# Kernel optimization log

Hardware: AMD Instinct MI355X
Metric: run time of the kernel (lower is better)

The kernel has to match this reference:

```python
import jax, jax.numpy as jnp
import numpy as np

N, E, H, HEADS, HD, L = 4096, 65536, 128, 4, 32, 4
NF, GF, EF, B = 16, 8, 4, 1


def _ln(x, g, b, eps=1e-5):
    mu = x.mean(-1, keepdims=True)
    v = ((x - mu) ** 2).mean(-1, keepdims=True)
    return (x - mu) * jax.lax.rsqrt(v + eps) * g + b


def _lin(x, W, b=None):
    y = x @ W.T
    return y if b is None else y + b


def _gelu(x):
    return jax.nn.gelu(x, approximate=False)


def setup_inputs() -> dict:
    key = jax.random.key(0)
    ks = iter(jax.random.split(key, 64))
    def rn(shape, s=0.05):
        return jax.random.normal(next(ks), shape, jnp.float32) * s
    inp = {}
    inp['x'] = jax.random.normal(next(ks), (N, NF), jnp.float32)
    inp['edge_index'] = jax.random.randint(next(ks), (2, E), 0, N, dtype=jnp.int32)
    inp['edge_attr'] = jax.random.normal(next(ks), (E, EF), jnp.float32)
    inp['u'] = jax.random.normal(next(ks), (1, GF), jnp.float32)
    inp['acting_mask'] = jax.random.randint(next(ks), (N,), 0, 2, dtype=jnp.int32).astype(bool)
    inp['h_tiles'] = jnp.zeros((N, H), jnp.float32)
    inp['batch'] = jnp.zeros((N,), jnp.int32)
    inp['turn_frac'] = jax.random.uniform(next(ks), (1,), jnp.float32)
    # node / global encoders
    inp['ne_W'] = rn((H, NF + 1)); inp['ne_b'] = jnp.zeros((H,)); inp['ne_g'] = jnp.ones((H,)); inp['ne_be'] = jnp.zeros((H,))
    inp['ge_W'] = rn((H, GF)); inp['ge_b'] = jnp.zeros((H,)); inp['ge_g'] = jnp.ones((H,)); inp['ge_be'] = jnp.zeros((H,))
    # GRUCell
    inp['gru_Wih'] = rn((3 * H, H)); inp['gru_bih'] = jnp.zeros((3 * H,))
    inp['gru_Whh'] = rn((3 * H, H)); inp['gru_bhh'] = jnp.zeros((3 * H,))
    # stacked GATv2 layers
    inp['gat_Wl'] = rn((L, H, H)); inp['gat_bl'] = jnp.zeros((L, H))
    inp['gat_Wr'] = rn((L, H, H)); inp['gat_br'] = jnp.zeros((L, H))
    inp['gat_We'] = rn((L, H, EF))
    inp['gat_att'] = rn((L, HEADS, HD))
    inp['gat_bias'] = jnp.zeros((L, H))
    inp['ln_g'] = jnp.ones((L, H)); inp['ln_b'] = jnp.zeros((L, H))
    # global MHA
    inp['attn_Win'] = rn((3 * H, H)); inp['attn_bin'] = jnp.zeros((3 * H,))
    inp['attn_Wout'] = rn((H, H)); inp['attn_bout'] = jnp.zeros((H,))
    inp['lng_g'] = jnp.ones((H,)); inp['lng_b'] = jnp.zeros((H,))
    # heads (edge_in = 2H + EF)
    inp['mv_W1'] = rn((H, 2 * H + EF)); inp['mv_b1'] = jnp.zeros((H,))
    inp['mv_W2'] = rn((1, H)); inp['mv_b2'] = jnp.zeros((1,))
    inp['fr_W1'] = rn((H, 2 * H + EF)); inp['fr_b1'] = jnp.zeros((H,))
    inp['fr_W2'] = rn((2, H)); inp['fr_b2'] = jnp.zeros((2,))
    inp['vl_W1'] = rn((H, 2 * H)); inp['vl_b1'] = jnp.zeros((H,))
    inp['vl_W2'] = rn((1, H)); inp['vl_b2'] = jnp.zeros((1,))
    return inp


def reference(x, edge_index, edge_attr, u, acting_mask, h_tiles, batch, turn_frac,
              ne_W, ne_b, ne_g, ne_be, ge_W, ge_b, ge_g, ge_be,
              gru_Wih, gru_bih, gru_Whh, gru_bhh,
              gat_Wl, gat_bl, gat_Wr, gat_br, gat_We, gat_att, gat_bias, ln_g, ln_b,
              attn_Win, attn_bin, attn_Wout, attn_bout, lng_g, lng_b,
              mv_W1, mv_b1, mv_W2, mv_b2, fr_W1, fr_b1, fr_W2, fr_b2,
              vl_W1, vl_b1, vl_W2, vl_b2):
    Nn = x.shape[0]
    src, dst = edge_index[0], edge_index[1]
    xa = jnp.concatenate([x, jnp.broadcast_to(turn_frac, (Nn, 1))], -1)
    h = _gelu(_ln(_lin(xa, ne_W, ne_b), ne_g, ne_be))
    ue = _gelu(_ln(_lin(u, ge_W, ge_b), ge_g, ge_be))
    h = h + ue[batch]
    # GRUCell (torch semantics)
    gi = _lin(h, gru_Wih, gru_bih)
    gh = _lin(h_tiles, gru_Whh, gru_bhh)
    i_r, i_z, i_n = jnp.split(gi, 3, -1)
    h_r, h_z, h_n = jnp.split(gh, 3, -1)
    r = jax.nn.sigmoid(i_r + h_r)
    z = jax.nn.sigmoid(i_z + h_z)
    n = jnp.tanh(i_n + r * h_n)
    h = (1.0 - z) * n + z * h_tiles
    h_tiles_new = jax.lax.stop_gradient(h)
    # stacked GATv2 message passing (eval mode: no dropout)
    for l in range(L):
        xl = _lin(h, gat_Wl[l], gat_bl[l]).reshape(Nn, HEADS, HD)   # source messages
        xr = _lin(h, gat_Wr[l], gat_br[l]).reshape(Nn, HEADS, HD)   # target
        ee = (edge_attr @ gat_We[l].T).reshape(-1, HEADS, HD)
        m = xl[src]                                                 # [E,heads,hd]
        s = jax.nn.leaky_relu(m + xr[dst] + ee, negative_slope=0.2)
        score = (s * gat_att[l]).sum(-1)                            # [E,heads]
        mx = jax.ops.segment_max(score, dst, num_segments=Nn)
        mx = jnp.where(jnp.isfinite(mx), mx, 0.0)
        ex = jnp.exp(score - mx[dst])
        den = jax.ops.segment_sum(ex, dst, num_segments=Nn)
        alpha_e = ex / (den[dst] + 1e-16)
        agg = jax.ops.segment_sum(alpha_e[..., None] * m, dst, num_segments=Nn)
        h_mp = agg.reshape(Nn, H) + gat_bias[l]
        h = _ln(h + h_mp, ln_g[l], ln_b[l])
    # global self-attention over all nodes as one sequence
    q, k, v = jnp.split(_lin(h, attn_Win, attn_bin), 3, -1)
    q = q.reshape(Nn, HEADS, HD); k = k.reshape(Nn, HEADS, HD); v = v.reshape(Nn, HEADS, HD)
    att = jax.nn.softmax(jnp.einsum('nhd,mhd->hnm', q, k) / np.float32(np.sqrt(HD)), axis=-1)
    ao = jnp.einsum('hnm,mhd->nhd', att, v).reshape(Nn, H)
    h = _ln(h + _lin(ao, attn_Wout, attn_bout), lng_g, lng_b)
    # edge heads
    eemb = jnp.concatenate([h[src], h[dst], edge_attr], -1)         # [E, 2H+EF]
    move_logits = _lin(_gelu(_lin(eemb, mv_W1, mv_b1)), mv_W2, mv_b2)[:, 0]
    fp = _lin(_gelu(_lin(eemb, fr_W1, fr_b1)), fr_W2, fr_b2)
    alpha = jax.nn.softplus(fp[:, 0]) + 1e-4
    beta = jax.nn.softplus(fp[:, 1]) + 1e-4
    # value head (global mean pool + masked acting pool)
    cnt = jax.ops.segment_sum(jnp.ones((Nn, 1), h.dtype), batch, num_segments=B)
    gpool = jax.ops.segment_sum(h, batch, num_segments=B) / cnt
    ah = jnp.where(acting_mask[:, None], h, 0.0)
    asum = jax.ops.segment_sum(ah, batch, num_segments=B) / cnt
    acnt = jnp.maximum(jax.ops.segment_sum(acting_mask[:, None].astype(h.dtype), batch, num_segments=B) / cnt, 1e-6)
    apool = asum / acnt
    vin = jnp.concatenate([gpool, apool], -1)
    value = _lin(_gelu(_lin(vin, vl_W1, vl_b1)), vl_W2, vl_b2)[:, 0]
    return move_logits, alpha, beta, value, h_tiles_new
```

## Files before the change

kernel.cpp:

```cpp
#include <hip/hip_runtime.h>
#include <math.h>


#define NN 4096
#define EE 65536
#define HH 128
#define NHEADS 4
#define HDIM 32
#define NLAYERS 4
#define NFEAT 16
#define GFEAT 8
#define EFEAT 4
#define KS 4
#define KPAD 296
#define XSTR 136
#define KSTR 40
#define VSTR 136

typedef short bf16x8 __attribute__((ext_vector_type(8)));
typedef float f32x4  __attribute__((ext_vector_type(4)));
union UB { uint4 u; bf16x8 v; };

__device__ __forceinline__ float gelu_f(float x){
  return 0.5f * x * (1.0f + erff(x * 0.7071067811865475f));
}
__device__ __forceinline__ float gelu_fast(float x){
  float u = x + 0.044715f * x * x * x;
  float t = __expf(-1.5957691216f * u);
  return x / (1.0f + t);
}
__device__ __forceinline__ float sigm_fast(float x){ return 1.0f / (1.0f + __expf(-x)); }
__device__ __forceinline__ float tanh_fast(float x){
  float t = __expf(-2.0f * fmaxf(x, -40.0f));
  return 1.0f - 2.0f * t / (1.0f + t);
}
__device__ __forceinline__ float softplus_f(float x){ return x > 20.0f ? x : log1pf(expf(x)); }
__device__ __forceinline__ unsigned short f2bf(float x){
  unsigned u = __float_as_uint(x);
  unsigned r = (u + 0x7FFFu + ((u >> 16) & 1u)) >> 16;
  return (unsigned short)r;
}
__device__ __forceinline__ float bf2f(unsigned short x){
  return __uint_as_float(((unsigned)x) << 16);
}
__device__ __forceinline__ unsigned pack2bf(float lo, float hi){
  unsigned a = (__float_as_uint(lo) + 0x8000u) >> 16;
  unsigned b = (__float_as_uint(hi) + 0x8000u) & 0xFFFF0000u;
  return a | b;
}

__device__ __forceinline__ float block_sum128(float v, float* red){
  int j = threadIdx.x;
  red[j] = v; __syncthreads();
  for (int s = 64; s > 0; s >>= 1){
    if (j < s) red[j] += red[j + s];
    __syncthreads();
  }
  float r = red[0];
  __syncthreads();
  return r;
}

__global__ void k_hist(const int* __restrict__ ei, int* __restrict__ cnt){
  int e = blockIdx.x * 256 + threadIdx.x;
  if (e < EE) atomicAdd(&cnt[ei[EE + e]], 1);
}

__global__ void k_scan(const int* __restrict__ cnt, int* __restrict__ off, int* __restrict__ cur){
  __shared__ int part[256];
  int t = threadIdx.x;
  int local[16];
  int s = 0;
  #pragma unroll
  for (int i = 0; i < 16; i++){ local[i] = s; s += cnt[t * 16 + i]; }
  part[t] = s; __syncthreads();
  for (int o = 1; o < 256; o <<= 1){
    int v = (t >= o) ? part[t - o] : 0;
    __syncthreads();
    part[t] += v;
    __syncthreads();
  }
  int base = part[t] - s;
  #pragma unroll
  for (int i = 0; i < 16; i++){ int o = base + local[i]; off[t * 16 + i] = o; cur[t * 16 + i] = o; }
  if (t == 255) off[NN] = part[255];
}

__global__ void k_scatter(const int* __restrict__ ei, const float* __restrict__ ea,
                          int* __restrict__ cur,
                          int* __restrict__ srcs, float* __restrict__ eas4){
  int e = blockIdx.x * 256 + threadIdx.x;
  if (e < EE){
    int d = ei[EE + e];
    int p = atomicAdd(&cur[d], 1);
    srcs[p] = ei[e];
    float4 a = *(const float4*)(ea + e * 4);
    *(float4*)(eas4 + p * 4) = a;
  }
}

__global__ void k_wprep(const float* __restrict__ Wih, const float* __restrict__ Whh,
                        const float* __restrict__ Wl, const float* __restrict__ Wr,
                        const float* __restrict__ Win, const float* __restrict__ Wout,
                        const float* __restrict__ tiles,
                        const float* __restrict__ bl, const float* __restrict__ br,
                        const float* __restrict__ ea,
                        const float* __restrict__ mvW1, const float* __restrict__ frW1,
                        unsigned short* __restrict__ wbuf, unsigned short* __restrict__ tilesb,
                        float* __restrict__ blrc,
                        unsigned short* __restrict__ wbE, unsigned short* __restrict__ eab,
                        int* __restrict__ cnt, float* __restrict__ gsum){
  int i = blockIdx.x * 256 + threadIdx.x;
  if (i < 49152){ wbuf[i] = f2bf(Wih[i]); }
  else if (i < 98304){ int j = i - 49152; wbuf[49152 + j] = f2bf(Whh[j]); }
  else if (i < 229376){
    int j = i - 98304;
    int l = j >> 15, rem = j & 32767, m = rem >> 7, k = rem & 127;
    float v = (m < 128) ? Wl[l * 16384 + m * 128 + k] : Wr[l * 16384 + (m - 128) * 128 + k];
    wbuf[98304 + j] = f2bf(v);
  }
  else if (i < 278528){ int j = i - 229376; wbuf[229376 + j] = f2bf(Win[j]); }
  else if (i < 294912){ int j = i - 278528; wbuf[278528 + j] = f2bf(Wout[j]); }
  else if (i < 819200){ int j = i - 294912; tilesb[j] = f2bf(tiles[j]); }
  else if (i < 820224){
    int j = i - 819200;
    int l = j >> 8, m = j & 255;
    blrc[j] = (m < 128) ? bl[l * 128 + m] : br[l * 128 + m - 128];
  }
  else if (i < 896000){
    int j = i - 820224;
    int n = j / KPAD, k = j - n * KPAD;
    float v = 0.0f;
    if (k < 2 * HH + EFEAT) v = (n < HH) ? mvW1[n * (2 * HH + EFEAT) + k]
                                         : frW1[(n - HH) * (2 * HH + EFEAT) + k];
    wbE[j] = f2bf(v);
  }
  else if (i < 1158144){
    int j = i - 896000;
    eab[j] = f2bf(ea[j]);
  }
  else if (i < 1162240){ cnt[i - 1158144] = 0; }
  else if (i < 1162497){ gsum[i - 1162240] = 0.0f; }
}

__device__ __forceinline__ void gemm_core(const unsigned short* __restrict__ Xb, int n0,
                                          const unsigned short* __restrict__ Wb, int m0,
                                          unsigned short* Xs, f32x4 acc[8]){
  int t = threadIdx.x;
  #pragma unroll
  for (int k2 = 0; k2 < 4; k2++){
    int v = t + k2 * 256;
    int r = v >> 4, c8 = v & 15;
    *(uint4*)(Xs + r * XSTR + c8 * 8) = *(const uint4*)(Xb + (n0 + r) * 128 + c8 * 8);
  }
  __syncthreads();
  int ln = t & 63, w = t >> 6, lm = ln & 15, quad = ln >> 4;
  const unsigned short* abase = Xs + (16 * w + lm) * XSTR + quad * 8;
  const unsigned short* bbase = Wb + (m0 + lm) * 128 + quad * 8;
  UB af[4];
  #pragma unroll
  for (int ks = 0; ks < 4; ks++) af[ks].u = *(const uint4*)(abase + ks * 32);
  #pragma unroll
  for (int i = 0; i < 8; i++) acc[i] = (f32x4){0.f, 0.f, 0.f, 0.f};
  #pragma unroll
  for (int t2 = 0; t2 < 8; t2++){
    #pragma unroll
    for (int ks = 0; ks < 4; ks++){
      UB bu;
      bu.u = *(const uint4*)(bbase + t2 * 16 * 128 + ks * 32);
      acc[t2] = __builtin_amdgcn_mfma_f32_16x16x32_bf16(af[ks].v, bu.v, acc[t2], 0, 0, 0);
    }
  }
}

__global__ __launch_bounds__(256) void k_gru_lin(const unsigned short* __restrict__ hb,
                                                 const unsigned short* __restrict__ tilesb,
                                                 const unsigned short* __restrict__ Wihb,
                                                 const unsigned short* __restrict__ Whhb,
                                                 const float* __restrict__ bih,
                                                 const float* __restrict__ bhh,
                                                 float* __restrict__ gi, float* __restrict__ gh){
  __shared__ __align__(16) unsigned short Xs[64 * XSTR];
  int z = blockIdx.z;
  const unsigned short* Xb = z ? tilesb : hb;
  const unsigned short* Wb = z ? Whhb : Wihb;
  const float* bias = z ? bhh : bih;
  float* Y = z ? gh : gi;
  int t = threadIdx.x;
  int n0 = blockIdx.x * 64, m0 = blockIdx.y * 128;
  f32x4 acc[8];
  gemm_core(Xb, n0, Wb, m0, Xs, acc);
  int ln = t & 63, w = t >> 6, lm = ln & 15, quad = ln >> 4;
  #pragma unroll
  for (int t2 = 0; t2 < 8; t2++){
    float bv = bias[m0 + t2 * 16 + lm];
    #pragma unroll
    for (int r = 0; r < 4; r++){
      Y[(n0 + 16 * w + quad * 4 + r) * 384 + m0 + t2 * 16 + lm] = acc[t2][r] + bv;
    }
  }
}

__global__ __launch_bounds__(256) void k_lin_gat(const unsigned short* __restrict__ Xb,
                                                 const unsigned short* __restrict__ Wb,
                                                 const float* __restrict__ bias,
                                                 unsigned short* __restrict__ Y){
  __shared__ __align__(16) unsigned short Xs[64 * XSTR];
  int t = threadIdx.x;
  int n0 = blockIdx.x * 64, m0 = blockIdx.y * 128;
  f32x4 acc[8];
  gemm_core(Xb, n0, Wb, m0, Xs, acc);
  int ln = t & 63, w = t >> 6, lm = ln & 15, quad = ln >> 4;
  #pragma unroll
  for (int t2 = 0; t2 < 8; t2++){
    float bv = bias[m0 + t2 * 16 + lm];
    #pragma unroll
    for (int r = 0; r < 4; r++){
      Y[(n0 + 16 * w + quad * 4 + r) * 256 + m0 + t2 * 16 + lm] = f2bf(acc[t2][r] + bv);
    }
  }
}

__global__ __launch_bounds__(256) void k_lin_qkv(const unsigned short* __restrict__ Xb,
                                                 const unsigned short* __restrict__ Wb,
                                                 const float* __restrict__ bias,
                                                 unsigned short* __restrict__ qb,
                                                 unsigned short* __restrict__ kb,
                                                 unsigned short* __restrict__ vt){
  __shared__ __align__(16) unsigned short Xs[64 * XSTR];
  int t = threadIdx.x;
  int n0 = blockIdx.x * 64, m0 = blockIdx.y * 128;
  f32x4 acc[8];
  gemm_core(Xb, n0, Wb, m0, Xs, acc);
  int ln = t & 63, w = t >> 6, lm = ln & 15, quad = ln >> 4;
  int nb = n0 + 16 * w + quad * 4;
  const float scale = 0.17677669529663687f;
  if (blockIdx.y == 0){
    #pragma unroll
    for (int t2 = 0; t2 < 8; t2++){
      int m = t2 * 16 + lm;
      float bv = bias[m];
      #pragma unroll
      for (int r = 0; r < 4; r++) qb[(nb + r) * HH + m] = f2bf(acc[t2][r] + bv);
    }
  } else if (blockIdx.y == 1){
    #pragma unroll
    for (int t2 = 0; t2 < 8; t2++){
      int m = t2 * 16 + lm;
      float bv = bias[128 + m];
      #pragma unroll
      for (int r = 0; r < 4; r++) kb[(nb + r) * HH + m] = f2bf((acc[t2][r] + bv) * scale);
    }
  } else {
    #pragma unroll
    for (int t2 = 0; t2 < 8; t2++){
      int m = t2 * 16 + lm;
      float bv = bias[256 + m];
      uint2 p;
      p.x = pack2bf(acc[t2][0] + bv, acc[t2][1] + bv);
      p.y = pack2bf(acc[t2][2] + bv, acc[t2][3] + bv);
      *(uint2*)(vt + m * NN + nb) = p;
    }
  }
}

__global__ void k_node_enc(const float* __restrict__ x, const float* __restrict__ tf,
                           const float* __restrict__ W, const float* __restrict__ b,
                           const float* __restrict__ g, const float* __restrict__ be,
                           const float* __restrict__ u, const float* __restrict__ geW,
                           const float* __restrict__ geb, const float* __restrict__ geg,
                           const float* __restrict__ gebe,
                           float* __restrict__ h, unsigned short* __restrict__ hb){
  __shared__ float red[128];
  __shared__ float xs[NFEAT + 1];
  __shared__ float us[GFEAT];
  int n = blockIdx.x, j = threadIdx.x;
  if (j < NFEAT) xs[j] = x[n * NFEAT + j];
  if (j == NFEAT) xs[NFEAT] = tf[0];
  if (j >= 32 && j < 32 + GFEAT) us[j - 32] = u[j - 32];
  __syncthreads();
  float ua = geb[j];
  #pragma unroll
  for (int k = 0; k < GFEAT; k++) ua += us[k] * geW[j * GFEAT + k];
  float umu = block_sum128(ua, red) * (1.0f / HH);
  float ud = ua - umu;
  float uvar = block_sum128(ud * ud, red) * (1.0f / HH);
  float uej = gelu_f(ud * rsqrtf(uvar + 1e-5f) * geg[j] + gebe[j]);
  float acc = b[j];
  #pragma unroll
  for (int k = 0; k < NFEAT + 1; k++) acc += xs[k] * W[j * (NFEAT + 1) + k];
  float mu = block_sum128(acc, red) * (1.0f / HH);
  float d = acc - mu;
  float var = block_sum128(d * d, red) * (1.0f / HH);
  float r = gelu_f(d * rsqrtf(var + 1e-5f) * g[j] + be[j]) + uej;
  h[n * HH + j] = r;
  hb[n * HH + j] = f2bf(r);
}

__global__ void k_gru_comb(const float* __restrict__ gi, const float* __restrict__ gh,
                           const float* __restrict__ tiles, float* __restrict__ h,
                           unsigned short* __restrict__ hb, float* __restrict__ out_tiles){
  int idx = blockIdx.x * 256 + threadIdx.x;
  int n = idx >> 7, j = idx & 127;
  float ir = gi[n * 384 + j], iz = gi[n * 384 + 128 + j], inn = gi[n * 384 + 256 + j];
  float hr = gh[n * 384 + j], hz = gh[n * 384 + 128 + j], hn = gh[n * 384 + 256 + j];
  float r = sigm_fast(ir + hr), z = sigm_fast(iz + hz);
  float nn2 = tanh_fast(inn + r * hn);
  float ts = tiles[idx];
  float hnew = (1.0f - z) * nn2 + z * ts;
  h[idx] = hnew;
  hb[idx] = f2bf(hnew);
  out_tiles[idx] = hnew;
}

__global__ __launch_bounds__(256) void k_gat_agg(
    const unsigned short* __restrict__ xlrb,
    const int* __restrict__ off, const int* __restrict__ srcs,
    const float* __restrict__ eas4,
    const float* __restrict__ We, const float* __restrict__ att,
    const float* __restrict__ bias, const float* __restrict__ g,
    const float* __restrict__ b, float* __restrict__ h,
    unsigned short* __restrict__ hb){
  int t = threadIdx.x, w = t >> 6, j = t & 63;
  int n = blockIdx.x * 4 + w;
  int p0 = off[n], p1 = off[n + 1];
  int c0 = 2 * j;
  float4 w0 = ((const float4*)We)[c0];
  float4 w1 = ((const float4*)We)[c0 + 1];
  float at0 = att[c0], at1 = att[c0 + 1];
  unsigned xr = *(const unsigned*)(xlrb + n * 256 + 128 + c0);
  float xr0 = bf2f((unsigned short)xr), xr1 = bf2f((unsigned short)(xr >> 16));
  float den = 0.f, a0 = 0.f, a1 = 0.f;
  int p = p0;
  for (; p + 4 <= p1; p += 4){
    int s0 = srcs[p], s1 = srcs[p + 1], s2 = srcs[p + 2], s3 = srcs[p + 3];
    unsigned x0 = *(const unsigned*)(xlrb + s0 * 256 + c0);
    unsigned x1 = *(const unsigned*)(xlrb + s1 * 256 + c0);
    unsigned x2 = *(const unsigned*)(xlrb + s2 * 256 + c0);
    unsigned x3 = *(const unsigned*)(xlrb + s3 * 256 + c0);
    float4 ev0 = *(const float4*)(eas4 + p * 4);
    float4 ev1 = *(const float4*)(eas4 + (p + 1) * 4);
    float4 ev2 = *(const float4*)(eas4 + (p + 2) * 4);
    float4 ev3 = *(const float4*)(eas4 + (p + 3) * 4);
    float x00 = bf2f((unsigned short)x0), x01 = bf2f((unsigned short)(x0 >> 16));
    float x10 = bf2f((unsigned short)x1), x11 = bf2f((unsigned short)(x1 >> 16));
    float x20 = bf2f((unsigned short)x2), x21 = bf2f((unsigned short)(x2 >> 16));
    float x30 = bf2f((unsigned short)x3), x31 = bf2f((unsigned short)(x3 >> 16));
    float vA0 = x00 + xr0 + ev0.x * w0.x + ev0.y * w0.y + ev0.z * w0.z + ev0.w * w0.w;
    float vA1 = x01 + xr1 + ev0.x * w1.x + ev0.y * w1.y + ev0.z * w1.z + ev0.w * w1.w;
    float vB0 = x10 + xr0 + ev1.x * w0.x + ev1.y * w0.y + ev1.z * w0.z + ev1.w * w0.w;
    float vB1 = x11 + xr1 + ev1.x * w1.x + ev1.y * w1.y + ev1.z * w1.z + ev1.w * w1.w;
    float vC0 = x20 + xr0 + ev2.x * w0.x + ev2.y * w0.y + ev2.z * w0.z + ev2.w * w0.w;
    float vC1 = x21 + xr1 + ev2.x * w1.x + ev2.y * w1.y + ev2.z * w1.z + ev2.w * w1.w;
    float vD0 = x30 + xr0 + ev3.x * w0.x + ev3.y * w0.y + ev3.z * w0.z + ev3.w * w0.w;
    float vD1 = x31 + xr1 + ev3.x * w1.x + ev3.y * w1.y + ev3.z * w1.z + ev3.w * w1.w;
    vA0 = vA0 > 0.f ? vA0 : 0.2f * vA0;  vA1 = vA1 > 0.f ? vA1 : 0.2f * vA1;
    vB0 = vB0 > 0.f ? vB0 : 0.2f * vB0;  vB1 = vB1 > 0.f ? vB1 : 0.2f * vB1;
    vC0 = vC0 > 0.f ? vC0 : 0.2f * vC0;  vC1 = vC1 > 0.f ? vC1 : 0.2f * vC1;
    vD0 = vD0 > 0.f ? vD0 : 0.2f * vD0;  vD1 = vD1 > 0.f ? vD1 : 0.2f * vD1;
    float sA = vA0 * at0 + vA1 * at1;
    float sB = vB0 * at0 + vB1 * at1;
    float sC = vC0 * at0 + vC1 * at1;
    float sD = vD0 * at0 + vD1 * at1;
    #pragma unroll
    for (int d = 1; d < 16; d <<= 1){
      sA += __shfl_xor(sA, d); sB += __shfl_xor(sB, d);
      sC += __shfl_xor(sC, d); sD += __shfl_xor(sD, d);
    }
    float eA = __expf(sA), eB = __expf(sB), eC = __expf(sC), eD = __expf(sD);
    den += (eA + eB) + (eC + eD);
    a0 += eA * x00 + eB * x10 + eC * x20 + eD * x30;
    a1 += eA * x01 + eB * x11 + eC * x21 + eD * x31;
  }
  for (; p < p1; p++){
    int s0 = srcs[p];
    float4 ev0 = *(const float4*)(eas4 + p * 4);
    unsigned x0 = *(const unsigned*)(xlrb + s0 * 256 + c0);
    float x00 = bf2f((unsigned short)x0), x01 = bf2f((unsigned short)(x0 >> 16));
    float vA0 = x00 + xr0 + ev0.x * w0.x + ev0.y * w0.y + ev0.z * w0.z + ev0.w * w0.w;
    float vA1 = x01 + xr1 + ev0.x * w1.x + ev0.y * w1.y + ev0.z * w1.z + ev0.w * w1.w;
    vA0 = vA0 > 0.f ? vA0 : 0.2f * vA0;  vA1 = vA1 > 0.f ? vA1 : 0.2f * vA1;
    float sA = vA0 * at0 + vA1 * at1;
    #pragma unroll
    for (int d = 1; d < 16; d <<= 1) sA += __shfl_xor(sA, d);
    float eA = __expf(sA);
    den += eA;
    a0 += eA * x00;
    a1 += eA * x01;
  }
  float dinv = 1.0f / (den + 1e-16f);
  float2 hv = *(const float2*)(h + n * HH + c0);
  float v0 = hv.x + a0 * dinv + bias[c0];
  float v1 = hv.y + a1 * dinv + bias[c0 + 1];
  float s = v0 + v1;
  #pragma unroll
  for (int d = 1; d < 64; d <<= 1) s += __shfl_xor(s, d);
  float mu = s * (1.0f / HH);
  float d0 = v0 - mu, d1 = v1 - mu;
  float q = d0 * d0 + d1 * d1;
  #pragma unroll
  for (int d = 1; d < 64; d <<= 1) q += __shfl_xor(q, d);
  float rstd = rsqrtf(q * (1.0f / HH) + 1e-5f);
  float o0 = d0 * rstd * g[c0] + b[c0];
  float o1 = d1 * rstd * g[c0 + 1] + b[c0 + 1];
  float2 ov; ov.x = o0; ov.y = o1;
  *(float2*)(h + n * HH + c0) = ov;
  unsigned pk = ((unsigned)f2bf(o0)) | (((unsigned)f2bf(o1)) << 16);
  *(unsigned*)(hb + n * HH + c0) = pk;
}

__global__ __launch_bounds__(256, 4) void k_attn_flash(
    const unsigned short* __restrict__ qb, const unsigned short* __restrict__ kb,
    const unsigned short* __restrict__ vt,
    float* __restrict__ pden, float* __restrict__ pacc){
  __shared__ __align__(16) unsigned short Kls[2][128 * KSTR];
  __shared__ __align__(16) unsigned short Vls[2][32 * VSTR];
  int t = threadIdx.x, w = t >> 6, ln = t & 63;
  int c = ln & 15, qd = ln >> 4;
  int hh = blockIdx.y, ks = blockIdx.z;
  int q0 = blockIdx.x * 64 + w * 16;
  UB qf; qf.u = *(const uint4*)(qb + (q0 + c) * HH + hh * HDIM + qd * 8);
  f32x4 o0a = {0,0,0,0}, o1a = {0,0,0,0}, o0b = {0,0,0,0}, o1b = {0,0,0,0};
  float denp = 0.f;
  int srcA = c + ((qd & 1) << 5);
  int srcB = srcA + 16;
  bool hi = qd >= 2;
  int kk2 = t >> 1, kp2 = (t & 1) * 2;
  int vr2 = t >> 3, vc2 = (t & 7) * 2;
  const unsigned short* kg = kb + hh * HDIM + kp2 * 8;
  const unsigned short* vg = vt + (hh * HDIM + vr2) * NN + vc2 * 8;

  auto stage = [&](int buf, int k0){
    uint4 ka = *(const uint4*)(kg + (k0 + kk2) * HH);
    uint4 kb4 = *(const uint4*)(kg + (k0 + kk2) * HH + 8);
    uint4 va = *(const uint4*)(vg + k0);
    uint4 vb4 = *(const uint4*)(vg + k0 + 8);
    *(uint4*)(&Kls[buf][kk2 * KSTR + kp2 * 8]) = ka;
    *(uint4*)(&Kls[buf][kk2 * KSTR + kp2 * 8 + 8]) = kb4;
    *(uint4*)(&Vls[buf][vr2 * VSTR + vc2 * 8]) = va;
    *(uint4*)(&Vls[buf][vr2 * VSTR + vc2 * 8 + 8]) = vb4;
  };
  auto comp = [&](int buf, int hs, f32x4& O0, f32x4& O1){
    UB kf0, kf1, vf0, vf1, pt;
    kf0.u = *(const uint4*)(&Kls[buf][(hs * 32 + c) * KSTR + qd * 8]);
    kf1.u = *(const uint4*)(&Kls[buf][(hs * 32 + 16 + c) * KSTR + qd * 8]);
    vf0.u = *(const uint4*)(&Vls[buf][c * VSTR + hs * 32 + qd * 8]);
    vf1.u = *(const uint4*)(&Vls[buf][(16 + c) * VSTR + hs * 32 + qd * 8]);
    f32x4 s0 = {0,0,0,0}, s1 = {0,0,0,0};
    s0 = __builtin_amdgcn_mfma_f32_16x16x32_bf16(kf0.v, qf.v, s0, 0, 0, 0);
    s1 = __builtin_amdgcn_mfma_f32_16x16x32_bf16(kf1.v, qf.v, s1, 0, 0, 0);
    float e00 = __expf(s0[0]), e01 = __expf(s0[1]), e02 = __expf(s0[2]), e03 = __expf(s0[3]);
    float e10 = __expf(s1[0]), e11 = __expf(s1[1]), e12 = __expf(s1[2]), e13 = __expf(s1[3]);
    denp += (e00 + e01) + (e02 + e03) + (e10 + e11) + (e12 + e13);
    int p00 = (int)pack2bf(e00, e01), p01 = (int)pack2bf(e02, e03);
    int p10 = (int)pack2bf(e10, e11), p11 = (int)pack2bf(e12, e13);
    int a00 = __shfl(p00, srcA), a01 = __shfl(p01, srcA);
    int b00 = __shfl(p00, srcB), b01 = __shfl(p01, srcB);
    int a10 = __shfl(p10, srcA), a11 = __shfl(p11, srcA);
    int b10 = __shfl(p10, srcB), b11 = __shfl(p11, srcB);
    pt.u.x = (unsigned)(hi ? a10 : a00);
    pt.u.y = (unsigned)(hi ? a11 : a01);
    pt.u.z = (unsigned)(hi ? b10 : b00);
    pt.u.w = (unsigned)(hi ? b11 : b01);
    O0 = __builtin_amdgcn_mfma_f32_16x16x32_bf16(vf0.v, pt.v, O0, 0, 0, 0);
    O1 = __builtin_amdgcn_mfma_f32_16x16x32_bf16(vf1.v, pt.v, O1, 0, 0, 0);
  };

  const int kbeg = ks * (NN / KS);
  const int NIT = (NN / KS) / 128;
  stage(0, kbeg);
  __syncthreads();
  for (int it = 0; it < NIT; it++){
    int buf = it & 1;
    if (it + 1 < NIT){
      int kn = kbeg + (it + 1) * 128;
      uint4 ka = *(const uint4*)(kg + (kn + kk2) * HH);
      uint4 kb4 = *(const uint4*)(kg + (kn + kk2) * HH + 8);
      uint4 va = *(const uint4*)(vg + kn);
      uint4 vb4 = *(const uint4*)(vg + kn + 8);
      comp(buf, 0, o0a, o1a);
      comp(buf, 1, o0b, o1b);
      comp(buf, 2, o0a, o1a);
      comp(buf, 3, o0b, o1b);
      *(uint4*)(&Kls[buf ^ 1][kk2 * KSTR + kp2 * 8]) = ka;
      *(uint4*)(&Kls[buf ^ 1][kk2 * KSTR + kp2 * 8 + 8]) = kb4;
      *(uint4*)(&Vls[buf ^ 1][vr2 * VSTR + vc2 * 8]) = va;
      *(uint4*)(&Vls[buf ^ 1][vr2 * VSTR + vc2 * 8 + 8]) = vb4;
    } else {
      comp(buf, 0, o0a, o1a);
      comp(buf, 1, o0b, o1b);
      comp(buf, 2, o0a, o1a);
      comp(buf, 3, o0b, o1b);
    }
    __syncthreads();
  }

  f32x4 o0 = o0a + o0b, o1 = o1a + o1b;
  denp += __shfl_xor(denp, 16);
  denp += __shfl_xor(denp, 32);
  int pi = ((q0 + c) * NHEADS + hh) * KS + ks;
  if (qd == 0) pden[pi] = denp;
  #pragma unroll
  for (int r = 0; r < 4; r++){
    pacc[pi * HDIM + qd * 4 + r]      = o0[r];
    pacc[pi * HDIM + 16 + qd * 4 + r] = o1[r];
  }
}

__global__ __launch_bounds__(256) void k_attn_out(
    const float* __restrict__ pden, const float* __restrict__ pacc,
    const unsigned short* __restrict__ Wb, const float* __restrict__ bout,
    const float* __restrict__ g, const float* __restrict__ b,
    const unsigned char* __restrict__ mask,
    float* __restrict__ h, unsigned short* __restrict__ hb,
    float* __restrict__ gsum, float* __restrict__ msum, float* __restrict__ mcnt){
  __shared__ __align__(16) unsigned short Xs[64 * XSTR];
  __shared__ float colg[128], colm[128], colc;
  int t = threadIdx.x;
  int n0 = blockIdx.x * 64;
  if (t < 128){ colg[t] = 0.f; colm[t] = 0.f; }
  if (t == 128) colc = 0.f;
  for (int idx = t; idx < 64 * 128; idx += 256){
    int r = idx >> 7, j = idx & 127;
    int n = n0 + r, hh = j >> 5, d = j & 31;
    float ds = 0.f, as = 0.f;
    #pragma unroll
    for (int ks2 = 0; ks2 < KS; ks2++){
      int pi = (n * NHEADS + hh) * KS + ks2;
      ds += pden[pi];
      as += pacc[pi * HDIM + d];
    }
    Xs[r * XSTR + j] = f2bf(as / ds);
  }
  __syncthreads();
  int ln = t & 63, w = t >> 6, lm = ln & 15, quad = ln >> 4;
  const unsigned short* abase = Xs + (16 * w + lm) * XSTR + quad * 8;
  const unsigned short* bbase = Wb + lm * 128 + quad * 8;
  UB af[4];
  #pragma unroll
  for (int ks2 = 0; ks2 < 4; ks2++) af[ks2].u = *(const uint4*)(abase + ks2 * 32);
  f32x4 acc[8];
  #pragma unroll
  for (int i = 0; i < 8; i++) acc[i] = (f32x4){0.f, 0.f, 0.f, 0.f};
  #pragma unroll
  for (int t2 = 0; t2 < 8; t2++){
    #pragma unroll
    for (int ks2 = 0; ks2 < 4; ks2++){
      UB bu;
      bu.u = *(const uint4*)(bbase + t2 * 16 * 128 + ks2 * 32);
      acc[t2] = __builtin_amdgcn_mfma_f32_16x16x32_bf16(af[ks2].v, bu.v, acc[t2], 0, 0, 0);
    }
  }
  int nb = n0 + 16 * w + quad * 4;
  float val[8][4];
  #pragma unroll
  for (int t2 = 0; t2 < 8; t2++){
    int m = t2 * 16 + lm;
    float bv = bout[m];
    #pragma unroll
    for (int r = 0; r < 4; r++)
      val[t2][r] = acc[t2][r] + bv + h[(nb + r) * HH + m];
  }
  float mu[4], rs[4];
  #pragma unroll
  for (int r = 0; r < 4; r++){
    float s = 0.f;
    #pragma unroll
    for (int t2 = 0; t2 < 8; t2++) s += val[t2][r];
    s += __shfl_xor(s, 1); s += __shfl_xor(s, 2);
    s += __shfl_xor(s, 4); s += __shfl_xor(s, 8);
    mu[r] = s * (1.0f / HH);
  }
  #pragma unroll
  for (int r = 0; r < 4; r++){
    float s = 0.f;
    #pragma unroll
    for (int t2 = 0; t2 < 8; t2++){ float d2 = val[t2][r] - mu[r]; s += d2 * d2; }
    s += __shfl_xor(s, 1); s += __shfl_xor(s, 2);
    s += __shfl_xor(s, 4); s += __shfl_xor(s, 8);
    rs[r] = rsqrtf(s * (1.0f / HH) + 1e-5f);
  }
  uchar4 mk = *(const uchar4*)(mask + nb);
  float mkf[4] = { mk.x ? 1.f : 0.f, mk.y ? 1.f : 0.f, mk.z ? 1.f : 0.f, mk.w ? 1.f : 0.f };
  #pragma unroll
  for (int t2 = 0; t2 < 8; t2++){
    int m = t2 * 16 + lm;
    float gm = g[m], bm = b[m];
    float sg = 0.f, sm = 0.f;
    #pragma unroll
    for (int r = 0; r < 4; r++){
      float o = (val[t2][r] - mu[r]) * rs[r] * gm + bm;
      h[(nb + r) * HH + m] = o;
      hb[(nb + r) * HH + m] = f2bf(o);
      sg += o;
      sm += mkf[r] * o;
    }
    sg += __shfl_xor(sg, 16); sg += __shfl_xor(sg, 32);
    sm += __shfl_xor(sm, 16); sm += __shfl_xor(sm, 32);
    if (quad == 0){
      atomicAdd(&colg[m], sg);
      atomicAdd(&colm[m], sm);
    }
  }
  if (lm == 0){
    float c = mkf[0] + mkf[1] + mkf[2] + mkf[3];
    atomicAdd(&colc, c);
  }
  __syncthreads();
  if (t < 128){
    atomicAdd(&gsum[t], colg[t]);
    atomicAdd(&msum[t], colm[t]);
  }
  if (t == 128) atomicAdd(mcnt, colc);
}

__global__ __launch_bounds__(256, 4) void k_edge_mfma(
    const unsigned short* __restrict__ hb, const unsigned short* __restrict__ eab,
    const int* __restrict__ ei, const unsigned short* __restrict__ wb,
    const float* __restrict__ mvb1, const float* __restrict__ frb1,
    const float* __restrict__ mvW2, const float* __restrict__ mvb2,
    const float* __restrict__ frW2, const float* __restrict__ frb2,
    float* __restrict__ out){
  __shared__ __align__(16) unsigned short As[64 * KPAD];
  __shared__ float am[64], a0[64], a1[64];
  int t = threadIdx.x;
  int e0 = blockIdx.x * 64;
  if (t < 64){ am[t] = 0.f; a0[t] = 0.f; a1[t] = 0.f; }
  {
    int el = t >> 2, p = t & 3;
    int e = e0 + el;
    int node = (p < 2) ? ei[e] : ei[EE + e];
    int half = p & 1;
    const uint4* srcp = (const uint4*)(hb + node * HH + half * 64);
    uint4* dstp = (uint4*)(As + el * KPAD + (p >> 1) * 128 + half * 64);
    #pragma unroll
    for (int i = 0; i < 8; i++) dstp[i] = srcp[i];
    if (p == 0){
      unsigned short* tail = As + el * KPAD + 256;
      tail[0] = eab[e * 4];     tail[1] = eab[e * 4 + 1];
      tail[2] = eab[e * 4 + 2]; tail[3] = eab[e * 4 + 3];
      #pragma unroll
      for (int i = 4; i < KPAD - 256; i++) tail[i] = 0;
    }
  }
  int ln = t & 63, w = t >> 6, lm = ln & 15, quad = ln >> 4;
  const unsigned short* bbase = wb + (w * 64 + lm) * KPAD + quad * 8;
  f32x4 acc[4][4];
  #pragma unroll
  for (int rt = 0; rt < 4; rt++)
    #pragma unroll
    for (int t2 = 0; t2 < 4; t2++) acc[rt][t2] = (f32x4){0.f, 0.f, 0.f, 0.f};
  __syncthreads();
  #pragma unroll
  for (int ks = 0; ks < 9; ks++){
    UB bf[4], af[4];
    #pragma unroll
    for (int t2 = 0; t2 < 4; t2++) bf[t2].u = *(const uint4*)(bbase + t2 * 16 * KPAD + ks * 32);
    #pragma unroll
    for (int rt = 0; rt < 4; rt++) af[rt].u = *(const uint4*)(As + (16 * rt + lm) * KPAD + quad * 8 + ks * 32);
    #pragma unroll
    for (int rt = 0; rt < 4; rt++)
      #pragma unroll
      for (int t2 = 0; t2 < 4; t2++)
        acc[rt][t2] = __builtin_amdgcn_mfma_f32_16x16x32_bf16(af[rt].v, bf[t2].v, acc[rt][t2], 0, 0, 0);
  }
  if (w < 2){
    #pragma unroll
    for (int rt = 0; rt < 4; rt++){
      #pragma unroll
      for (int r = 0; r < 4; r++){
        float s = 0.f;
        #pragma unroll
        for (int t2 = 0; t2 < 4; t2++){
          int n = w * 64 + t2 * 16 + lm;
          s += gelu_fast(acc[rt][t2][r] + mvb1[n]) * mvW2[n];
        }
        #pragma unroll
        for (int d = 1; d < 16; d <<= 1) s += __shfl_xor(s, d);
        if (lm == 0) atomicAdd(&am[16 * rt + 4 * quad + r], s);
      }
    }
  } else {
    #pragma unroll
    for (int rt = 0; rt < 4; rt++){
      #pragma unroll
      for (int r = 0; r < 4; r++){
        float s0 = 0.f, s1 = 0.f;
        #pragma unroll
        for (int t2 = 0; t2 < 4; t2++){
          int n = (w - 2) * 64 + t2 * 16 + lm;
          float g = gelu_fast(acc[rt][t2][r] + frb1[n]);
          s0 += g * frW2[n];
          s1 += g * frW2[128 + n];
        }
        #pragma unroll
        for (int d = 1; d < 16; d <<= 1){ s0 += __shfl_xor(s0, d); s1 += __shfl_xor(s1, d); }
        if (lm == 0){
          atomicAdd(&a0[16 * rt + 4 * quad + r], s0);
          atomicAdd(&a1[16 * rt + 4 * quad + r], s1);
        }
      }
    }
  }
  __syncthreads();
  if (t < 64){
    int e = e0 + t;
    out[e]          = am[t] + mvb2[0];
    out[EE + e]     = softplus_f(a0[t] + frb2[0]) + 1e-4f;
    out[2 * EE + e] = softplus_f(a1[t] + frb2[1]) + 1e-4f;
  }
}

__global__ void k_value(const float* __restrict__ gsum, const float* __restrict__ msum,
                        const float* __restrict__ mcnt,
                        const float* __restrict__ W1, const float* __restrict__ b1,
                        const float* __restrict__ W2, const float* __restrict__ b2,
                        float* __restrict__ out_val){
  __shared__ float red[128];
  __shared__ float vin[256];
  int j = threadIdx.x;
  float gp = gsum[j] * (1.0f / NN);
  float as = msum[j] * (1.0f / NN);
  float ac = fmaxf(mcnt[0] * (1.0f / NN), 1e-6f);
  vin[j] = gp; vin[HH + j] = as / ac;
  __syncthreads();
  float acc = b1[j];
  const float* w = &W1[j * 256];
  #pragma unroll 4
  for (int k = 0; k < 256; k++) acc += vin[k] * w[k];
  float hv = gelu_f(acc) * W2[j];
  float s = block_sum128(hv, red);
  if (j == 0) out_val[0] = s + b2[0];
}

extern "C" void kernel_launch(void* const* d_in, const int* in_sizes, int n_in,
                              void* d_out, int out_size, void* d_ws, size_t ws_size,
                              hipStream_t stream){
  (void)in_sizes; (void)n_in; (void)out_size; (void)ws_size;
  const float* x        = (const float*)d_in[0];
  const int*   ei       = (const int*)d_in[1];
  const float* ea       = (const float*)d_in[2];
  const float* u        = (const float*)d_in[3];
  const unsigned char* mask = (const unsigned char*)d_in[4];
  const float* tiles    = (const float*)d_in[5];
  const float* tf       = (const float*)d_in[7];
  const float* ne_W  = (const float*)d_in[8];
  const float* ne_b  = (const float*)d_in[9];
  const float* ne_g  = (const float*)d_in[10];
  const float* ne_be = (const float*)d_in[11];
  const float* ge_W  = (const float*)d_in[12];
  const float* ge_b  = (const float*)d_in[13];
  const float* ge_g  = (const float*)d_in[14];
  const float* ge_be = (const float*)d_in[15];
  const float* gru_Wih = (const float*)d_in[16];
  const float* gru_bih = (const float*)d_in[17];
  const float* gru_Whh = (const float*)d_in[18];
  const float* gru_bhh = (const float*)d_in[19];
  const float* gat_Wl  = (const float*)d_in[20];
  const float* gat_bl  = (const float*)d_in[21];
  const float* gat_Wr  = (const float*)d_in[22];
  const float* gat_br  = (const float*)d_in[23];
  const float* gat_We  = (const float*)d_in[24];
  const float* gat_att = (const float*)d_in[25];
  const float* gat_bias= (const float*)d_in[26];
  const float* ln_g    = (const float*)d_in[27];
  const float* ln_b    = (const float*)d_in[28];
  const float* attn_Win = (const float*)d_in[29];
  const float* attn_bin = (const float*)d_in[30];
  const float* attn_Wout= (const float*)d_in[31];
  const float* attn_bout= (const float*)d_in[32];
  const float* lng_g    = (const float*)d_in[33];
  const float* lng_b    = (const float*)d_in[34];
  const float* mv_W1 = (const float*)d_in[35];
  const float* mv_b1 = (const float*)d_in[36];
  const float* mv_W2 = (const float*)d_in[37];
  const float* mv_b2 = (const float*)d_in[38];
  const float* fr_W1 = (const float*)d_in[39];
  const float* fr_b1 = (const float*)d_in[40];
  const float* fr_W2 = (const float*)d_in[41];
  const float* fr_b2 = (const float*)d_in[42];
  const float* vl_W1 = (const float*)d_in[43];
  const float* vl_b1 = (const float*)d_in[44];
  const float* vl_W2 = (const float*)d_in[45];
  const float* vl_b2 = (const float*)d_in[46];

  float* ws = (float*)d_ws;
  float* h      = ws;
  float* xlr    = ws + 524288;
  unsigned short* hb     = (unsigned short*)(ws + 1572864);
  unsigned short* tilesb = (unsigned short*)(ws + 1835008);
  unsigned short* wbuf   = (unsigned short*)(ws + 2097152);
  unsigned short* Wihb  = wbuf;
  unsigned short* Whhb  = wbuf + 49152;
  unsigned short* Wlrb  = wbuf + 98304;
  unsigned short* Winb  = wbuf + 229376;
  unsigned short* Woutb = wbuf + 278528;
  float* blrc   = ws + 2244608;
  float* gsum   = ws + 2245760;
  float* msum   = ws + 2245888;
  float* mcnt   = ws + 2246016;
  int*   cnt    = (int*)(ws + 2246032);
  int*   off    = cnt + NN;
  int*   cur    = off + NN + 1;
  unsigned short* eab = (unsigned short*)(ws + 2323904);
  unsigned short* wbE = (unsigned short*)(ws + 2454976);
  float* S      = ws + 2492864;
  float* gi = S;
  float* gh = S + 1572864;
  float* eas4 = S;
  int*   srcs = (int*)(S + 262144);
  unsigned short* xlrb = (unsigned short*)xlr;
  unsigned short* qb = (unsigned short*)xlr;
  unsigned short* kb = (unsigned short*)(xlr + 262144);
  unsigned short* vt = (unsigned short*)(xlr + 524288 + 16384);
  float* pacc = S + 327680;
  float* pden = S + 327680 + 2097152;

  float* out       = (float*)d_out;
  float* out_val   = out + 3 * EE;
  float* out_tiles = out + 3 * EE + 1;

  k_wprep<<<(1162497 + 255) / 256, 256, 0, stream>>>(gru_Wih, gru_Whh, gat_Wl, gat_Wr,
                                                     attn_Win, attn_Wout, tiles,
                                                     gat_bl, gat_br, ea, mv_W1, fr_W1,
                                                     wbuf, tilesb, blrc, wbE, eab,
                                                     cnt, gsum);

  k_node_enc<<<NN, 128, 0, stream>>>(x, tf, ne_W, ne_b, ne_g, ne_be,
                                     u, ge_W, ge_b, ge_g, ge_be, h, hb);

  { dim3 g(NN / 64, 3, 2);
    k_gru_lin<<<g, 256, 0, stream>>>(hb, tilesb, Wihb, Whhb, gru_bih, gru_bhh, gi, gh); }
  k_gru_comb<<<NN * HH / 256, 256, 0, stream>>>(gi, gh, tiles, h, hb, out_tiles);

  k_hist   <<<EE / 256, 256, 0, stream>>>(ei, cnt);
  k_scan   <<<1, 256, 0, stream>>>(cnt, off, cur);
  k_scatter<<<EE / 256, 256, 0, stream>>>(ei, ea, cur, srcs, eas4);

  for (int l = 0; l < NLAYERS; l++){
    { dim3 g(NN / 64, 2);
      k_lin_gat<<<g, 256, 0, stream>>>(hb, Wlrb + l * 32768, blrc + l * 256, xlrb); }
    k_gat_agg<<<NN / 4, 256, 0, stream>>>(xlrb, off, srcs, eas4,
                                          gat_We + l * HH * EFEAT,
                                          gat_att + l * NHEADS * HDIM,
                                          gat_bias + l * HH, ln_g + l * HH, ln_b + l * HH,
                                          h, hb);
  }

  { dim3 g(NN / 64, 3);
    k_lin_qkv<<<g, 256, 0, stream>>>(hb, Winb, attn_bin, qb, kb, vt); }
  { dim3 gattn(NN / 64, NHEADS, KS);
    k_attn_flash<<<gattn, 256, 0, stream>>>(qb, kb, vt, pden, pacc); }
  k_attn_out<<<NN / 64, 256, 0, stream>>>(pden, pacc, Woutb, attn_bout, lng_g, lng_b,
                                          mask, h, hb, gsum, msum, mcnt);

  k_edge_mfma<<<EE / 64, 256, 0, stream>>>(hb, eab, ei, wbE, mv_b1, fr_b1,
                                           mv_W2, mv_b2, fr_W2, fr_b2, out);

  k_value<<<1, 128, 0, stream>>>(gsum, msum, mcnt, vl_W1, vl_b1, vl_W2, vl_b2, out_val);
}
```

Baseline: 354.2 us.

## Merge small kernels into neighbours to cut launch count

Folds the node encoder into the weight-prep kernel as extra blocks that each handle two nodes, and folds the edge histogram into the GRU combine kernel. The value head becomes one extra block of the edge MLP kernel. It also uses readfirstlane for the CSR offsets in GAT aggregation. Together these drop three kernel launches and the gaps between them. The risk is more branching and more shared memory in the fused kernels, which could lower occupancy in the edge kernel.

```diff
diff --git a/kernel.cpp b/kernel.cpp
--- a/kernel.cpp
+++ b/kernel.cpp
@@ -16,6 +16,7 @@
 #define XSTR 136
 #define KSTR 40
 #define VSTR 136
+#define WPB 4541
 
 typedef short bf16x8 __attribute__((ext_vector_type(8)));
 typedef float f32x4  __attribute__((ext_vector_type(4)));
@@ -47,23 +48,6 @@
   unsigned a = (__float_as_uint(lo) + 0x8000u) >> 16;
   unsigned b = (__float_as_uint(hi) + 0x8000u) & 0xFFFF0000u;
   return a | b;
-}
-
-__device__ __forceinline__ float block_sum128(float v, float* red){
-  int j = threadIdx.x;
-  red[j] = v; __syncthreads();
-  for (int s = 64; s > 0; s >>= 1){
-    if (j < s) red[j] += red[j + s];
-    __syncthreads();
-  }
-  float r = red[0];
-  __syncthreads();
-  return r;
-}
-
-__global__ void k_hist(const int* __restrict__ ei, int* __restrict__ cnt){
-  int e = blockIdx.x * 256 + threadIdx.x;
-  if (e < EE) atomicAdd(&cnt[ei[EE + e]], 1);
 }
 
 __global__ void k_scan(const int* __restrict__ cnt, int* __restrict__ off, int* __restrict__ cur){
@@ -99,48 +83,98 @@
   }
 }
 
-__global__ void k_wprep(const float* __restrict__ Wih, const float* __restrict__ Whh,
-                        const float* __restrict__ Wl, const float* __restrict__ Wr,
-                        const float* __restrict__ Win, const float* __restrict__ Wout,
-                        const float* __restrict__ tiles,
-                        const float* __restrict__ bl, const float* __restrict__ br,
-                        const float* __restrict__ ea,
-                        const float* __restrict__ mvW1, const float* __restrict__ frW1,
-                        unsigned short* __restrict__ wbuf, unsigned short* __restrict__ tilesb,
-                        float* __restrict__ blrc,
-                        unsigned short* __restrict__ wbE, unsigned short* __restrict__ eab,
-                        int* __restrict__ cnt, float* __restrict__ gsum){
-  int i = blockIdx.x * 256 + threadIdx.x;
-  if (i < 49152){ wbuf[i] = f2bf(Wih[i]); }
-  else if (i < 98304){ int j = i - 49152; wbuf[49152 + j] = f2bf(Whh[j]); }
-  else if (i < 229376){
-    int j = i - 98304;
-    int l = j >> 15, rem = j & 32767, m = rem >> 7, k = rem & 127;
-    float v = (m < 128) ? Wl[l * 16384 + m * 128 + k] : Wr[l * 16384 + (m - 128) * 128 + k];
-    wbuf[98304 + j] = f2bf(v);
-  }
-  else if (i < 278528){ int j = i - 229376; wbuf[229376 + j] = f2bf(Win[j]); }
-  else if (i < 294912){ int j = i - 278528; wbuf[278528 + j] = f2bf(Wout[j]); }
-  else if (i < 819200){ int j = i - 294912; tilesb[j] = f2bf(tiles[j]); }
-  else if (i < 820224){
-    int j = i - 819200;
-    int l = j >> 8, m = j & 255;
-    blrc[j] = (m < 128) ? bl[l * 128 + m] : br[l * 128 + m - 128];
-  }
-  else if (i < 896000){
-    int j = i - 820224;
-    int n = j / KPAD, k = j - n * KPAD;
-    float v = 0.0f;
-    if (k < 2 * HH + EFEAT) v = (n < HH) ? mvW1[n * (2 * HH + EFEAT) + k]
-                                         : frW1[(n - HH) * (2 * HH + EFEAT) + k];
-    wbE[j] = f2bf(v);
-  }
-  else if (i < 1158144){
-    int j = i - 896000;
-    eab[j] = f2bf(ea[j]);
-  }
-  else if (i < 1162240){ cnt[i - 1158144] = 0; }
-  else if (i < 1162497){ gsum[i - 1162240] = 0.0f; }
+__global__ void k_wprep_enc(const float* __restrict__ Wih, const float* __restrict__ Whh,
+                            const float* __restrict__ Wl, const float* __restrict__ Wr,
+                            const float* __restrict__ Win, const float* __restrict__ Wout,
+                            const float* __restrict__ tiles,
+                            const float* __restrict__ bl, const float* __restrict__ br,
+                            const float* __restrict__ ea,
+                            const float* __restrict__ mvW1, const float* __restrict__ frW1,
+                            unsigned short* __restrict__ wbuf, unsigned short* __restrict__ tilesb,
+                            float* __restrict__ blrc,
+                            unsigned short* __restrict__ wbE, unsigned short* __restrict__ eab,
+                            int* __restrict__ cnt, float* __restrict__ gsum,
+                            const float* __restrict__ x, const float* __restrict__ tf,
+                            const float* __restrict__ neW, const float* __restrict__ neb,
+                            const float* __restrict__ neg, const float* __restrict__ nebe,
+                            const float* __restrict__ u, const float* __restrict__ geW,
+                            const float* __restrict__ geb, const float* __restrict__ geg,
+                            const float* __restrict__ gebe,
+                            float* __restrict__ h, unsigned short* __restrict__ hb){
+  int t = threadIdx.x;
+  if (blockIdx.x < WPB){
+    int i = blockIdx.x * 256 + t;
+    if (i < 49152){ wbuf[i] = f2bf(Wih[i]); }
+    else if (i < 98304){ int j = i - 49152; wbuf[49152 + j] = f2bf(Whh[j]); }
+    else if (i < 229376){
+      int j = i - 98304;
+      int l = j >> 15, rem = j & 32767, m = rem >> 7, k = rem & 127;
+      float v = (m < 128) ? Wl[l * 16384 + m * 128 + k] : Wr[l * 16384 + (m - 128) * 128 + k];
+      wbuf[98304 + j] = f2bf(v);
+    }
+    else if (i < 278528){ int j = i - 229376; wbuf[229376 + j] = f2bf(Win[j]); }
+    else if (i < 294912){ int j = i - 278528; wbuf[278528 + j] = f2bf(Wout[j]); }
+    else if (i < 819200){ int j = i - 294912; tilesb[j] = f2bf(tiles[j]); }
+    else if (i < 820224){
+      int j = i - 819200;
+      int l = j >> 8, m = j & 255;
+      blrc[j] = (m < 128) ? bl[l * 128 + m] : br[l * 128 + m - 128];
+    }
+    else if (i < 896000){
+      int j = i - 820224;
+      int n = j / KPAD, k = j - n * KPAD;
+      float v = 0.0f;
+      if (k < 2 * HH + EFEAT) v = (n < HH) ? mvW1[n * (2 * HH + EFEAT) + k]
+                                           : frW1[(n - HH) * (2 * HH + EFEAT) + k];
+      wbE[j] = f2bf(v);
+    }
+    else if (i < 1158144){
+      int j = i - 896000;
+      eab[j] = f2bf(ea[j]);
+    }
+    else if (i < 1162240){ cnt[i - 1158144] = 0; }
+    else if (i < 1162497){ gsum[i - 1162240] = 0.0f; }
+    return;
+  }
+  __shared__ float red[256];
+  __shared__ float xs[2][NFEAT + 1];
+  __shared__ float us[GFEAT];
+  int nb = blockIdx.x - WPB;
+  int half = t >> 7, j = t & 127;
+  int n = nb * 2 + half;
+  if (j < NFEAT) xs[half][j] = x[n * NFEAT + j];
+  if (j == NFEAT) xs[half][NFEAT] = tf[0];
+  if (t < GFEAT) us[t] = u[t];
+  __syncthreads();
+  int rb = half * 128;
+  float ua = geb[j];
+  #pragma unroll
+  for (int k = 0; k < GFEAT; k++) ua += us[k] * geW[j * GFEAT + k];
+  red[rb + j] = ua; __syncthreads();
+  #pragma unroll
+  for (int s = 64; s > 0; s >>= 1){ if (j < s) red[rb + j] += red[rb + j + s]; __syncthreads(); }
+  float umu = red[rb] * (1.0f / HH); __syncthreads();
+  float ud = ua - umu;
+  red[rb + j] = ud * ud; __syncthreads();
+  #pragma unroll
+  for (int s = 64; s > 0; s >>= 1){ if (j < s) red[rb + j] += red[rb + j + s]; __syncthreads(); }
+  float uvar = red[rb] * (1.0f / HH); __syncthreads();
+  float uej = gelu_f(ud * rsqrtf(uvar + 1e-5f) * geg[j] + gebe[j]);
+  float acc = neb[j];
+  #pragma unroll
+  for (int k = 0; k < NFEAT + 1; k++) acc += xs[half][k] * neW[j * (NFEAT + 1) + k];
+  red[rb + j] = acc; __syncthreads();
+  #pragma unroll
+  for (int s = 64; s > 0; s >>= 1){ if (j < s) red[rb + j] += red[rb + j + s]; __syncthreads(); }
+  float mu = red[rb] * (1.0f / HH); __syncthreads();
+  float d = acc - mu;
+  red[rb + j] = d * d; __syncthreads();
+  #pragma unroll
+  for (int s = 64; s > 0; s >>= 1){ if (j < s) red[rb + j] += red[rb + j + s]; __syncthreads(); }
+  float var = red[rb] * (1.0f / HH);
+  float r = gelu_f(d * rsqrtf(var + 1e-5f) * neg[j] + nebe[j]) + uej;
+  h[n * HH + j] = r;
+  hb[n * HH + j] = f2bf(r);
 }
 
 __device__ __forceinline__ void gemm_core(const unsigned short* __restrict__ Xb, int n0,
@@ -264,43 +298,17 @@
   }
 }
 
-__global__ void k_node_enc(const float* __restrict__ x, const float* __restrict__ tf,
-                           const float* __restrict__ W, const float* __restrict__ b,
-                           const float* __restrict__ g, const float* __restrict__ be,
-                           const float* __restrict__ u, const float* __restrict__ geW,
-                           const float* __restrict__ geb, const float* __restrict__ geg,
-                           const float* __restrict__ gebe,
-                           float* __restrict__ h, unsigned short* __restrict__ hb){
-  __shared__ float red[128];
-  __shared__ float xs[NFEAT + 1];
-  __shared__ float us[GFEAT];
-  int n = blockIdx.x, j = threadIdx.x;
-  if (j < NFEAT) xs[j] = x[n * NFEAT + j];
-  if (j == NFEAT) xs[NFEAT] = tf[0];
-  if (j >= 32 && j < 32 + GFEAT) us[j - 32] = u[j - 32];
-  __syncthreads();
-  float ua = geb[j];
-  #pragma unroll
-  for (int k = 0; k < GFEAT; k++) ua += us[k] * geW[j * GFEAT + k];
-  float umu = block_sum128(ua, red) * (1.0f / HH);
-  float ud = ua - umu;
-  float uvar = block_sum128(ud * ud, red) * (1.0f / HH);
-  float uej = gelu_f(ud * rsqrtf(uvar + 1e-5f) * geg[j] + gebe[j]);
-  float acc = b[j];
-  #pragma unroll
-  for (int k = 0; k < NFEAT + 1; k++) acc += xs[k] * W[j * (NFEAT + 1) + k];
-  float mu = block_sum128(acc, red) * (1.0f / HH);
-  float d = acc - mu;
-  float var = block_sum128(d * d, red) * (1.0f / HH);
-  float r = gelu_f(d * rsqrtf(var + 1e-5f) * g[j] + be[j]) + uej;
-  h[n * HH + j] = r;
-  hb[n * HH + j] = f2bf(r);
-}
-
 __global__ void k_gru_comb(const float* __restrict__ gi, const float* __restrict__ gh,
                            const float* __restrict__ tiles, float* __restrict__ h,
-                           unsigned short* __restrict__ hb, float* __restrict__ out_tiles){
-  int idx = blockIdx.x * 256 + threadIdx.x;
+                           unsigned short* __restrict__ hb, float* __restrict__ out_tiles,
+                           const int* __restrict__ ei, int* __restrict__ cnt){
+  int bid = blockIdx.x, t = threadIdx.x;
+  if (bid >= NN * HH / 256){
+    int e = (bid - NN * HH / 256) * 256 + t;
+    if (e < EE) atomicAdd(&cnt[ei[EE + e]], 1);
+    return;
+  }
+  int idx = bid * 256 + t;
   int n = idx >> 7, j = idx & 127;
   float ir = gi[n * 384 + j], iz = gi[n * 384 + 128 + j], inn = gi[n * 384 + 256 + j];
   float hr = gh[n * 384 + j], hz = gh[n * 384 + 128 + j], hn = gh[n * 384 + 256 + j];
@@ -323,7 +331,8 @@
     unsigned short* __restrict__ hb){
   int t = threadIdx.x, w = t >> 6, j = t & 63;
   int n = blockIdx.x * 4 + w;
-  int p0 = off[n], p1 = off[n + 1];
+  int p0 = __builtin_amdgcn_readfirstlane(off[n]);
+  int p1 = __builtin_amdgcn_readfirstlane(off[n + 1]);
   int c0 = 2 * j;
   float4 w0 = ((const float4*)We)[c0];
   float4 w1 = ((const float4*)We)[c0 + 1];
@@ -620,10 +629,43 @@
     const float* __restrict__ mvb1, const float* __restrict__ frb1,
     const float* __restrict__ mvW2, const float* __restrict__ mvb2,
     const float* __restrict__ frW2, const float* __restrict__ frb2,
-    float* __restrict__ out){
+    const float* __restrict__ gsum, const float* __restrict__ msum,
+    const float* __restrict__ mcnt,
+    const float* __restrict__ vlW1, const float* __restrict__ vlb1,
+    const float* __restrict__ vlW2, const float* __restrict__ vlb2,
+    float* __restrict__ out, float* __restrict__ out_val){
   __shared__ __align__(16) unsigned short As[64 * KPAD];
   __shared__ float am[64], a0[64], a1[64];
+  __shared__ float red[128];
+  __shared__ float vin[256];
   int t = threadIdx.x;
+  if (blockIdx.x == EE / 64){
+    int j = t & 127;
+    if (t < 128){
+      float gp = gsum[j] * (1.0f / NN);
+      float as2 = msum[j] * (1.0f / NN);
+      float ac = fmaxf(mcnt[0] * (1.0f / NN), 1e-6f);
+      vin[j] = gp; vin[HH + j] = as2 / ac;
+    }
+    __syncthreads();
+    float hv = 0.f;
+    if (t < 128){
+      float acc2 = vlb1[j];
+      const float* wv = &vlW1[j * 256];
+      #pragma unroll 4
+      for (int k = 0; k < 256; k++) acc2 += vin[k] * wv[k];
+      hv = gelu_f(acc2) * vlW2[j];
+    }
+    if (t < 128) red[j] = hv;
+    __syncthreads();
+    #pragma unroll
+    for (int s = 64; s > 0; s >>= 1){
+      if (t < s) red[t] += red[t + s];
+      __syncthreads();
+    }
+    if (t == 0) out_val[0] = red[0] + vlb2[0];
+    return;
+  }
   int e0 = blockIdx.x * 64;
   if (t < 64){ am[t] = 0.f; a0[t] = 0.f; a1[t] = 0.f; }
   {
@@ -709,28 +751,6 @@
     out[EE + e]     = softplus_f(a0[t] + frb2[0]) + 1e-4f;
     out[2 * EE + e] = softplus_f(a1[t] + frb2[1]) + 1e-4f;
   }
-}
-
-__global__ void k_value(const float* __restrict__ gsum, const float* __restrict__ msum,
-                        const float* __restrict__ mcnt,
-                        const float* __restrict__ W1, const float* __restrict__ b1,
-                        const float* __restrict__ W2, const float* __restrict__ b2,
-                        float* __restrict__ out_val){
-  __shared__ float red[128];
-  __shared__ float vin[256];
-  int j = threadIdx.x;
-  float gp = gsum[j] * (1.0f / NN);
-  float as = msum[j] * (1.0f / NN);
-  float ac = fmaxf(mcnt[0] * (1.0f / NN), 1e-6f);
-  vin[j] = gp; vin[HH + j] = as / ac;
-  __syncthreads();
-  float acc = b1[j];
-  const float* w = &W1[j * 256];
-  #pragma unroll 4
-  for (int k = 0; k < 256; k++) acc += vin[k] * w[k];
-  float hv = gelu_f(acc) * W2[j];
-  float s = block_sum128(hv, red);
-  if (j == 0) out_val[0] = s + b2[0];
 }
 
 extern "C" void kernel_launch(void* const* d_in, const int* in_sizes, int n_in,
@@ -820,20 +840,18 @@
   float* out_val   = out + 3 * EE;
   float* out_tiles = out + 3 * EE + 1;
 
-  k_wprep<<<(1162497 + 255) / 256, 256, 0, stream>>>(gru_Wih, gru_Whh, gat_Wl, gat_Wr,
-                                                     attn_Win, attn_Wout, tiles,
-                                                     gat_bl, gat_br, ea, mv_W1, fr_W1,
-                                                     wbuf, tilesb, blrc, wbE, eab,
-                                                     cnt, gsum);
-
-  k_node_enc<<<NN, 128, 0, stream>>>(x, tf, ne_W, ne_b, ne_g, ne_be,
-                                     u, ge_W, ge_b, ge_g, ge_be, h, hb);
+  k_wprep_enc<<<WPB + NN / 2, 256, 0, stream>>>(gru_Wih, gru_Whh, gat_Wl, gat_Wr,
+                                                attn_Win, attn_Wout, tiles,
+                                                gat_bl, gat_br, ea, mv_W1, fr_W1,
+                                                wbuf, tilesb, blrc, wbE, eab,
+                                                cnt, gsum,
+                                                x, tf, ne_W, ne_b, ne_g, ne_be,
+                                                u, ge_W, ge_b, ge_g, ge_be, h, hb);
 
   { dim3 g(NN / 64, 3, 2);
     k_gru_lin<<<g, 256, 0, stream>>>(hb, tilesb, Wihb, Whhb, gru_bih, gru_bhh, gi, gh); }
-  k_gru_comb<<<NN * HH / 256, 256, 0, stream>>>(gi, gh, tiles, h, hb, out_tiles);
-
-  k_hist   <<<EE / 256, 256, 0, stream>>>(ei, cnt);
+  k_gru_comb<<<NN * HH / 256 + EE / 256, 256, 0, stream>>>(gi, gh, tiles, h, hb, out_tiles,
+                                                           ei, cnt);
   k_scan   <<<1, 256, 0, stream>>>(cnt, off, cur);
   k_scatter<<<EE / 256, 256, 0, stream>>>(ei, ea, cur, srcs, eas4);
 
@@ -854,8 +872,9 @@
   k_attn_out<<<NN / 64, 256, 0, stream>>>(pden, pacc, Woutb, attn_bout, lng_g, lng_b,
                                           mask, h, hb, gsum, msum, mcnt);
 
-  k_edge_mfma<<<EE / 64, 256, 0, stream>>>(hb, eab, ei, wbE, mv_b1, fr_b1,
-                                           mv_W2, mv_b2, fr_W2, fr_b2, out);
-
-  k_value<<<1, 128, 0, stream>>>(gsum, msum, mcnt, vl_W1, vl_b1, vl_W2, vl_b2, out_val);
-}
+  k_edge_mfma<<<EE / 64 + 1, 256, 0, stream>>>(hb, eab, ei, wbE, mv_b1, fr_b1,
+                                               mv_W2, mv_b2, fr_W2, fr_b2,
+                                               gsum, msum, mcnt,
+                                               vl_W1, vl_b1, vl_W2, vl_b2,
+                                               out, out_val);
+}
```

Result: faster. 339.8 us, median of 2 (-4.1%).
